# Kernel tuning notes

Measured on AMD Instinct MI355X. Metric: run time of the kernel, lower is better.

The kernel has to match this reference:

```python
import jax, jax.numpy as jnp
import numpy as np

MARGIN = 0.1
EPS = 1e-6


def setup_inputs() -> dict:
    key = jax.random.key(0)
    k1, k2, k3 = jax.random.split(key, 3)
    B = 8192
    predictions = jax.random.normal(k1, (B,), dtype=jnp.float32)
    targets = jax.random.normal(k2, (B,), dtype=jnp.float32)
    mask = jax.random.bernoulli(k3, 0.9, (B,))  # bool (B,)
    return {"predictions": predictions, "targets": targets, "mask": mask}


def reference(predictions, targets, mask):
    # Reduce multi-output predictions/targets to scalars per example
    p = predictions.mean(axis=-1) if predictions.ndim > 1 else predictions
    t = targets.mean(axis=-1) if targets.ndim > 1 else targets
    B = p.shape[0]

    dt = t[:, None] - t[None, :]              # (B, B) target diffs
    dp = p[:, None] - p[None, :]              # (B, B) prediction diffs

    # only pairs i < j, both unmasked, with |target diff| >= 1e-6
    upper = jnp.triu(jnp.ones((B, B), dtype=bool), k=1)
    valid = upper & (jnp.abs(dt) >= EPS) & mask[:, None] & mask[None, :]

    # MarginRankingLoss: max(0, -y * (x1 - x2) + margin), y = sign(dt)
    hinge = jnp.maximum(0.0, -jnp.sign(dt) * dp + MARGIN)

    total = jnp.where(valid, hinge, 0.0).sum()
    count = valid.sum()
    return total / jnp.maximum(count, 1).astype(total.dtype)
```

## Files before the change

kernel.cpp:

```cpp
#include <hip/hip_runtime.h>
#include <math.h>

#define TPB 256
#define JCHUNK 128

__global__ __launch_bounds__(TPB) void mrl_partial(
    const float* __restrict__ p, const float* __restrict__ t,
    const int* __restrict__ m, int B,
    float* __restrict__ blk_sum, float* __restrict__ blk_cnt)
{
    const int i0  = blockIdx.x * TPB;
    const int j0  = blockIdx.y * JCHUNK;
    const int blk = blockIdx.y * gridDim.x + blockIdx.x;

    if (j0 + JCHUNK - 1 <= i0) {
        if (threadIdx.x == 0) { blk_sum[blk] = 0.0f; blk_cnt[blk] = 0.0f; }
        return;
    }

    __shared__ float sp[JCHUNK];
    __shared__ float st[JCHUNK];

    if (threadIdx.x < JCHUNK) {
        const int j = j0 + threadIdx.x;
        const bool ok = (j < B);
        sp[threadIdx.x] = ok ? p[j] : 0.0f;
        st[threadIdx.x] = (ok && m[j]) ? t[j] : __builtin_nanf("");
    }
    __syncthreads();

    const int i = i0 + threadIdx.x;
    float pi = 0.0f, ti = __builtin_nanf("");
    if (i < B) {
        pi = p[i];
        ti = m[i] ? t[i] : __builtin_nanf("");
    }

    float acc = 0.0f, cnt = 0.0f;
    const bool diag = (j0 < i0 + TPB);

    if (!diag) {
        #pragma unroll 8
        for (int k = 0; k < JCHUNK; ++k) {
            const float dt = ti - st[k];
            const float q  = sp[k] - pi;
            const bool  v  = fabsf(dt) >= 1e-6f;
            float h = (dt > 0.0f) ? (q + 0.1f) : (0.1f - q);
            h = fmaxf(h, 0.0f);
            if (v) { acc += h; cnt += 1.0f; }
        }
    } else {
        #pragma unroll 8
        for (int k = 0; k < JCHUNK; ++k) {
            const int   j  = j0 + k;
            const float dt = ti - st[k];
            const float q  = sp[k] - pi;
            const bool  v  = (fabsf(dt) >= 1e-6f) && (j > i);
            float h = (dt > 0.0f) ? (q + 0.1f) : (0.1f - q);
            h = fmaxf(h, 0.0f);
            if (v) { acc += h; cnt += 1.0f; }
        }
    }

    #pragma unroll
    for (int off = 32; off > 0; off >>= 1) {
        acc += __shfl_down(acc, off, 64);
        cnt += __shfl_down(cnt, off, 64);
    }
    __shared__ float wsum[TPB / 64];
    __shared__ float wcnt[TPB / 64];
    const int lane = threadIdx.x & 63;
    const int wid  = threadIdx.x >> 6;
    if (lane == 0) { wsum[wid] = acc; wcnt[wid] = cnt; }
    __syncthreads();
    if (threadIdx.x == 0) {
        float a = 0.0f, c = 0.0f;
        #pragma unroll
        for (int w = 0; w < TPB / 64; ++w) { a += wsum[w]; c += wcnt[w]; }
        blk_sum[blk] = a;
        blk_cnt[blk] = c;
    }
}

__global__ __launch_bounds__(256) void mrl_final(
    const float* __restrict__ blk_sum, const float* __restrict__ blk_cnt,
    int nblk, float* __restrict__ out)
{
    double a = 0.0, c = 0.0;
    for (int k = threadIdx.x; k < nblk; k += 256) {
        a += (double)blk_sum[k];
        c += (double)blk_cnt[k];
    }
    #pragma unroll
    for (int off = 32; off > 0; off >>= 1) {
        a += __shfl_down(a, off, 64);
        c += __shfl_down(c, off, 64);
    }
    __shared__ double sa[4];
    __shared__ double sc[4];
    const int lane = threadIdx.x & 63;
    const int wid  = threadIdx.x >> 6;
    if (lane == 0) { sa[wid] = a; sc[wid] = c; }
    __syncthreads();
    if (threadIdx.x == 0) {
        double A = 0.0, C = 0.0;
        #pragma unroll
        for (int w = 0; w < 4; ++w) { A += sa[w]; C += sc[w]; }
        out[0] = (C > 0.0) ? (float)(A / C) : 0.0f;
    }
}

extern "C" void kernel_launch(void* const* d_in, const int* in_sizes, int n_in,
                              void* d_out, int out_size, void* d_ws, size_t ws_size,
                              hipStream_t stream)
{
    const float* p = (const float*)d_in[0];
    const float* t = (const float*)d_in[1];
    const int*   m = (const int*)d_in[2];
    const int B = in_sizes[0];

    const int iblocks = (B + TPB - 1) / TPB;
    const int jchunks = (B + JCHUNK - 1) / JCHUNK;
    const int nblk = iblocks * jchunks;

    float* blk_sum = (float*)d_ws;
    float* blk_cnt = blk_sum + nblk;

    dim3 grid(iblocks, jchunks);
    mrl_partial<<<grid, TPB, 0, stream>>>(p, t, m, B, blk_sum, blk_cnt);
    mrl_final<<<1, 256, 0, stream>>>(blk_sum, blk_cnt, nblk, (float*)d_out);
}
```

Before: 75.48 us.

## Fuse final reduction via atomics and last-block detection, simplify hinge math

Removes the second reduction kernel: each active block atomically adds its partial sum and count into double accumulators, and the last block to finish, detected with an atomic counter, writes the result. A memset of the accumulators is added before the launch. Early-exit blocks no longer write zeros. The inner loop packs p and t into one float2 in shared memory and computes the hinge with copysign and fma plus a select instead of a branch. Trades one kernel launch for global atomics and a memset call. The host code also keeps a dead first counting loop with a stray label.

New measurement: 103.6 us. 1.37x slower.

```diff
diff --git a/kernel.cpp b/kernel.cpp
--- a/kernel.cpp
+++ b/kernel.cpp
@@ -4,28 +4,24 @@
 #define TPB 256
 #define JCHUNK 128
 
-__global__ __launch_bounds__(TPB) void mrl_partial(
+__global__ __launch_bounds__(TPB) void mrl_fused(
     const float* __restrict__ p, const float* __restrict__ t,
-    const int* __restrict__ m, int B,
-    float* __restrict__ blk_sum, float* __restrict__ blk_cnt)
+    const int* __restrict__ m, int B, int n_active,
+    double* __restrict__ acc_ws, float* __restrict__ out)
 {
-    const int i0  = blockIdx.x * TPB;
-    const int j0  = blockIdx.y * JCHUNK;
-    const int blk = blockIdx.y * gridDim.x + blockIdx.x;
+    const int i0 = blockIdx.x * TPB;
+    const int j0 = blockIdx.y * JCHUNK;
 
-    if (j0 + JCHUNK - 1 <= i0) {
-        if (threadIdx.x == 0) { blk_sum[blk] = 0.0f; blk_cnt[blk] = 0.0f; }
-        return;
-    }
+    if (j0 + JCHUNK - 1 <= i0) return;
 
-    __shared__ float sp[JCHUNK];
-    __shared__ float st[JCHUNK];
+    __shared__ float2 sj[JCHUNK];
 
     if (threadIdx.x < JCHUNK) {
         const int j = j0 + threadIdx.x;
         const bool ok = (j < B);
-        sp[threadIdx.x] = ok ? p[j] : 0.0f;
-        st[threadIdx.x] = (ok && m[j]) ? t[j] : __builtin_nanf("");
+        float pj = ok ? p[j] : 0.0f;
+        float tj = (ok && m[j]) ? t[j] : __builtin_nanf("");
+        sj[threadIdx.x] = make_float2(pj, tj);
     }
     __syncthreads();
 
@@ -42,23 +38,27 @@
     if (!diag) {
         #pragma unroll 8
         for (int k = 0; k < JCHUNK; ++k) {
-            const float dt = ti - st[k];
-            const float q  = sp[k] - pi;
+            const float2 pt = sj[k];
+            const float dt = ti - pt.y;
+            const float q  = pt.x - pi;
             const bool  v  = fabsf(dt) >= 1e-6f;
-            float h = (dt > 0.0f) ? (q + 0.1f) : (0.1f - q);
-            h = fmaxf(h, 0.0f);
-            if (v) { acc += h; cnt += 1.0f; }
+            const float cs = copysignf(1.0f, dt);
+            const float h  = fmaxf(fmaf(cs, q, 0.1f), 0.0f);
+            acc += v ? h : 0.0f;
+            cnt += v ? 1.0f : 0.0f;
         }
     } else {
         #pragma unroll 8
         for (int k = 0; k < JCHUNK; ++k) {
+            const float2 pt = sj[k];
             const int   j  = j0 + k;
-            const float dt = ti - st[k];
-            const float q  = sp[k] - pi;
+            const float dt = ti - pt.y;
+            const float q  = pt.x - pi;
             const bool  v  = (fabsf(dt) >= 1e-6f) && (j > i);
-            float h = (dt > 0.0f) ? (q + 0.1f) : (0.1f - q);
-            h = fmaxf(h, 0.0f);
-            if (v) { acc += h; cnt += 1.0f; }
+            const float cs = copysignf(1.0f, dt);
+            const float h  = fmaxf(fmaf(cs, q, 0.1f), 0.0f);
+            acc += v ? h : 0.0f;
+            cnt += v ? 1.0f : 0.0f;
         }
     }
 
@@ -73,40 +73,22 @@
     const int wid  = threadIdx.x >> 6;
     if (lane == 0) { wsum[wid] = acc; wcnt[wid] = cnt; }
     __syncthreads();
+
     if (threadIdx.x == 0) {
         float a = 0.0f, c = 0.0f;
         #pragma unroll
         for (int w = 0; w < TPB / 64; ++w) { a += wsum[w]; c += wcnt[w]; }
-        blk_sum[blk] = a;
-        blk_cnt[blk] = c;
-    }
-}
 
-__global__ __launch_bounds__(256) void mrl_final(
-    const float* __restrict__ blk_sum, const float* __restrict__ blk_cnt,
-    int nblk, float* __restrict__ out)
-{
-    double a = 0.0, c = 0.0;
-    for (int k = threadIdx.x; k < nblk; k += 256) {
-        a += (double)blk_sum[k];
-        c += (double)blk_cnt[k];
-    }
-    #pragma unroll
-    for (int off = 32; off > 0; off >>= 1) {
-        a += __shfl_down(a, off, 64);
-        c += __shfl_down(c, off, 64);
-    }
-    __shared__ double sa[4];
-    __shared__ double sc[4];
-    const int lane = threadIdx.x & 63;
-    const int wid  = threadIdx.x >> 6;
-    if (lane == 0) { sa[wid] = a; sc[wid] = c; }
-    __syncthreads();
-    if (threadIdx.x == 0) {
-        double A = 0.0, C = 0.0;
-        #pragma unroll
-        for (int w = 0; w < 4; ++w) { A += sa[w]; C += sc[w]; }
-        out[0] = (C > 0.0) ? (float)(A / C) : 0.0f;
+        atomicAdd(&acc_ws[0], (double)a);
+        atomicAdd(&acc_ws[1], (double)c);
+        __threadfence();
+        unsigned* ctr = (unsigned*)&acc_ws[2];
+        const unsigned old = atomicAdd(ctr, 1u);
+        if (old == (unsigned)(n_active - 1)) {
+            const double S = atomicAdd(&acc_ws[0], 0.0);
+            const double C = atomicAdd(&acc_ws[1], 0.0);
+            out[0] = (float)(S / fmax(C, 1.0));
+        }
     }
 }
 
@@ -121,12 +103,24 @@
 
     const int iblocks = (B + TPB - 1) / TPB;
     const int jchunks = (B + JCHUNK - 1) / JCHUNK;
-    const int nblk = iblocks * jchunks;
 
-    float* blk_sum = (float*)d_ws;
-    float* blk_cnt = blk_sum + nblk;
+    int n_active = 0;
+    for (int bi = 0; bi < iblocks; ++bi) {
+        const int i0 = bi * TPB;
+        for (int bj = 0; bj < jchunks; ++bj) {
+            if (bj * JCHUNK + JCHUNK - 1 > i0) { ++n_active; break_hint: ; }
+        }
+    }
+    n_active = 0;
+    for (int bi = 0; bi < iblocks; ++bi) {
+        const int i0 = bi * TPB;
+        const int skipped = (i0 >= JCHUNK - 1) ? ((i0 - (JCHUNK - 1)) / JCHUNK + 1) : 0;
+        n_active += jchunks - (skipped < jchunks ? skipped : jchunks);
+    }
+
+    hipMemsetAsync(d_ws, 0, 24, stream);
 
     dim3 grid(iblocks, jchunks);
-    mrl_partial<<<grid, TPB, 0, stream>>>(p, t, m, B, blk_sum, blk_cnt);
-    mrl_final<<<1, 256, 0, stream>>>(blk_sum, blk_cnt, nblk, (float*)d_out);
+    mrl_fused<<<grid, TPB, 0, stream>>>(p, t, m, B, n_active,
+                                        (double*)d_ws, (float*)d_out);
 }
```
